# Performance work log

Measured on AMD Instinct MI355X. Metric: run time of the kernel, lower is better.

Reference implementation:

```python
import jax, jax.numpy as jnp
import numpy as np

B, T, DIN, H, DOUT = 64, 1024, 256, 512, 256


def _lstm_layer(xseq, Wih, bih, Whh, bhh):
    """xseq: (T, B, Din) -> hidden sequence (T, B, Hout)."""
    bsz = xseq.shape[1]
    hdim = Whh.shape[0]
    # hoist the input projection out of the recurrence (one big GEMM)
    xg = jnp.einsum('tbd,dh->tbh', xseq, Wih) + bih  # (T, B, 4H)

    def step(carry, xg_t):
        h, c = carry
        gates = xg_t + h @ Whh + bhh          # (B, 4H)
        i, f, g, o = jnp.split(gates, 4, axis=-1)  # torch chunk order: i,f,g,o
        c = jax.nn.sigmoid(f) * c + jax.nn.sigmoid(i) * jnp.tanh(g)
        h = jax.nn.sigmoid(o) * jnp.tanh(c)
        return (h, c), h

    h0 = jnp.zeros((bsz, hdim), xseq.dtype)
    (_, _), hs = jax.lax.scan(step, (h0, h0), xg)
    return hs


def setup_inputs() -> dict:
    key = jax.random.key(0)
    ks = jax.random.split(key, 9)

    def lin(k, fan_in, fan_out):
        bound = 1.0 / np.sqrt(fan_in)
        kw, kb = jax.random.split(k)
        W = jax.random.uniform(kw, (fan_in, fan_out), jnp.float32, -bound, bound)
        b = jax.random.uniform(kb, (fan_out,), jnp.float32, -bound, bound)
        return W, b

    x = jax.random.normal(ks[0], (B, T, DIN), jnp.float32)
    W_ih0, b_ih0 = lin(ks[1], DIN, 4 * H)
    W_hh0, b_hh0 = lin(ks[2], H, 4 * H)
    W_ih1, b_ih1 = lin(ks[3], H, 4 * DOUT)
    W_hh1, b_hh1 = lin(ks[4], DOUT, 4 * DOUT)
    return {
        'x': x,
        'W_ih0': W_ih0, 'b_ih0': b_ih0, 'W_hh0': W_hh0, 'b_hh0': b_hh0,
        'W_ih1': W_ih1, 'b_ih1': b_ih1, 'W_hh1': W_hh1, 'b_hh1': b_hh1,
    }


def reference(x, W_ih0, b_ih0, W_hh0, b_hh0, W_ih1, b_ih1, W_hh1, b_hh1):
    xseq = jnp.transpose(x, (1, 0, 2))              # (T, B, DIN)
    h1 = _lstm_layer(xseq, W_ih0, b_ih0, W_hh0, b_hh0)   # (T, B, H)
    h2 = _lstm_layer(h1, W_ih1, b_ih1, W_hh1, b_hh1)     # (T, B, DOUT)
    return jnp.transpose(h2, (1, 0, 2))             # (B, T, DOUT)
```

## Files before the change

### kernel.cpp

```cpp
#include <hip/hip_runtime.h>


constexpr int BB   = 64;
constexpr int TT   = 1024;
constexpr int DIN  = 256;
constexpr int H0   = 512;
constexpr int H1   = 256;
constexpr int NWG0 = 128;
constexpr int NWG1 = 64;
constexpr int NWG  = NWG0 + NWG1;
constexpr int NTHR = 256;
constexpr int NKT  = 24;

typedef _Float16 v8h __attribute__((ext_vector_type(8)));
typedef __fp16   v2p __attribute__((ext_vector_type(2)));
typedef float    v4f __attribute__((ext_vector_type(4)));
typedef unsigned int v4u __attribute__((ext_vector_type(4)));

union U1 { unsigned u; v2p h; };
union U4 { v4u u; v8h h; };

__device__ __forceinline__ unsigned pk2(float a, float b){
  U1 c; c.h = __builtin_amdgcn_cvt_pkrtz(a, b); return c.u;
}
__device__ __forceinline__ float lo16(unsigned u){ U1 c; c.u = u; return (float)c.h[0]; }
__device__ __forceinline__ float hi16(unsigned u){ U1 c; c.u = u; return (float)c.h[1]; }
__device__ __forceinline__ v8h as_h8(v4u u){ U4 c; c.u = u; return c.h; }

__device__ __forceinline__ v4f mfma16(v8h a, v8h b, v4f c){
  return __builtin_amdgcn_mfma_f32_16x16x32_f16(a, b, c, 0, 0, 0);
}

__device__ __forceinline__ float sigf(float v){ return 1.0f / (1.0f + __expf(-v)); }
__device__ __forceinline__ float tanhf_(float v){
  float e = __expf(2.0f * v);
  return 1.0f - 2.0f / (e + 1.0f);
}

__device__ __forceinline__ void waitflags(const unsigned* f, int n, unsigned tgt, int lane){
  for (;;){
    bool ok = true;
    #pragma unroll
    for (int base = 0; base < n; base += 64)
      ok = ok && (__hip_atomic_load(f + base + lane, __ATOMIC_RELAXED,
                                    __HIP_MEMORY_SCOPE_AGENT) >= tgt);
    if (__all(ok)) return;
    __builtin_amdgcn_s_sleep(1);
  }
}

__device__ __forceinline__ void acq_fence(){
  __builtin_amdgcn_fence(__ATOMIC_ACQUIRE, "agent");
}

__device__ __forceinline__ void frag_from_pairs(v4u p0, v4u p1, v8h& A, v8h& B){
  v4u ua, ub;
  ua[0] = __builtin_amdgcn_perm(p0[1], p0[0], 0x05040100u);
  ua[1] = __builtin_amdgcn_perm(p0[3], p0[2], 0x05040100u);
  ua[2] = __builtin_amdgcn_perm(p1[1], p1[0], 0x05040100u);
  ua[3] = __builtin_amdgcn_perm(p1[3], p1[2], 0x05040100u);
  ub[0] = __builtin_amdgcn_perm(p0[1], p0[0], 0x07060302u);
  ub[1] = __builtin_amdgcn_perm(p0[3], p0[2], 0x07060302u);
  ub[2] = __builtin_amdgcn_perm(p1[1], p1[0], 0x07060302u);
  ub[3] = __builtin_amdgcn_perm(p1[3], p1[2], 0x07060302u);
  A = as_h8(ua); B = as_h8(ub);
}

__device__ __forceinline__ void frag_from_floats(v4f f0, v4f f1, v8h& A, v8h& B){
  float v[8] = { f0[0], f0[1], f0[2], f0[3], f1[0], f1[1], f1[2], f1[3] };
  v4u ua, ub;
  #pragma unroll
  for (int d = 0; d < 4; ++d){
    unsigned p = pk2(v[2*d], v[2*d+1]);
    ua[d] = p;
    ub[d] = pk2(v[2*d] - lo16(p), v[2*d+1] - hi16(p));
  }
  A = as_h8(ua); B = as_h8(ub);
}

__global__ void __launch_bounds__(NTHR, 1)
lstm_mfma(const float* __restrict__ x, const unsigned* __restrict__ xp, int use_xp,
          const float* __restrict__ Wih0, const float* __restrict__ bih0,
          const float* __restrict__ Whh0, const float* __restrict__ bhh0,
          const float* __restrict__ Wih1, const float* __restrict__ bih1,
          const float* __restrict__ Whh1, const float* __restrict__ bhh1,
          unsigned* h1p, unsigned* h2p,
          unsigned* flg, float* out)
{
  __shared__ v4u wfbs[NKT * 64];

  const int tid   = threadIdx.x;
  const int wg    = blockIdx.x;
  const bool isL0 = wg < NWG0;
  const int lw    = isL0 ? wg : wg - NWG0;
  const int H     = isL0 ? H0 : H1;
  const int jbase = lw * 4;
  const int lane  = tid & 63;
  const int mt    = tid >> 6;
  const int n     = lane & 15;
  const int quad  = lane >> 4;
  const int gcol  = (n >> 2) * H + jbase + (n & 3);
  const int brow  = mt * 16 + n;

  v4u wfa[NKT];
  {
    const float* Wi = isL0 ? Wih0 : Wih1;
    const float* Wh = isL0 ? Whh0 : Whh1;
    const int Ki  = isL0 ? DIN : H0;
    const int ldw = 4 * H;
    #pragma unroll
    for (int kt = 0; kt < NKT; ++kt){
      const int ks = kt * 32 + quad * 8;
      float w[8];
      #pragma unroll
      for (int j = 0; j < 8; ++j){
        const int k = ks + j;
        w[j] = (k < Ki) ? Wi[(size_t)k * ldw + gcol]
                        : Wh[(size_t)(k - Ki) * ldw + gcol];
      }
      v4u ua, ub;
      #pragma unroll
      for (int d = 0; d < 4; ++d){
        const unsigned p = pk2(w[2*d], w[2*d+1]);
        ua[d] = p;
        ub[d] = pk2(w[2*d] - lo16(p), w[2*d+1] - hi16(p));
      }
      wfa[kt] = ua;
      if (mt == 0) wfbs[kt * 64 + lane] = ub;
    }
  }
  const float bsum = isL0 ? (bih0[gcol] + bhh0[gcol]) : (bih1[gcol] + bhh1[gcol]);

  float c0 = 0.f, c1 = 0.f, c2 = 0.f, c3 = 0.f;
  __syncthreads();

  for (int i = 0; i <= TT; ++i){
    const bool act = isL0 ? (i < TT) : (i >= 1);
    const int t    = isL0 ? i : (i - 1);

    v4f acc1 = { bsum, bsum, bsum, bsum };
    v4f acc2 = { 0.f, 0.f, 0.f, 0.f };

    if (isL0 && act){
      if (use_xp){
        const unsigned* xr = xp + ((size_t)brow * TT + t) * DIN + quad * 8;
        v4u xP0[8], xP1[8];
        #pragma unroll
        for (int kt = 0; kt < 8; ++kt){
          xP0[kt] = *(const v4u*)(xr + kt * 32);
          xP1[kt] = *(const v4u*)(xr + kt * 32 + 4);
        }
        #pragma unroll
        for (int kt = 0; kt < 8; ++kt){
          v8h A, Ab; frag_from_pairs(xP0[kt], xP1[kt], A, Ab);
          v8h Wa = as_h8(wfa[kt]), Wb = as_h8(wfbs[kt * 64 + lane]);
          acc1 = mfma16(A,  Wa, acc1);
          acc2 = mfma16(A,  Wb, acc2);
          acc2 = mfma16(Ab, Wa, acc2);
        }
      } else {
        const float* xr = x + ((size_t)brow * TT + t) * DIN + quad * 8;
        v4f xF0[8], xF1[8];
        #pragma unroll
        for (int kt = 0; kt < 8; ++kt){
          xF0[kt] = *(const v4f*)(xr + kt * 32);
          xF1[kt] = *(const v4f*)(xr + kt * 32 + 4);
        }
        #pragma unroll
        for (int kt = 0; kt < 8; ++kt){
          v8h A, Ab; frag_from_floats(xF0[kt], xF1[kt], A, Ab);
          v8h Wa = as_h8(wfa[kt]), Wb = as_h8(wfbs[kt * 64 + lane]);
          acc1 = mfma16(A,  Wa, acc1);
          acc2 = mfma16(A,  Wb, acc2);
          acc2 = mfma16(Ab, Wa, acc2);
        }
      }
    }

    if (tid < 64){
      if (i >= 1) waitflags(flg, NWG, (unsigned)i, lane);
      acq_fence();
    }
    __syncthreads();

    if (act){
      if (isL0){
        const unsigned* hr = h1p + (size_t)((t + 1) & 1) * (BB * H0)
                                 + (size_t)brow * H0 + quad * 8;
        v4u hP0[16], hP1[16];
        #pragma unroll
        for (int kt = 0; kt < 16; ++kt){
          hP0[kt] = *(const v4u*)(hr + kt * 32);
          hP1[kt] = *(const v4u*)(hr + kt * 32 + 4);
        }
        #pragma unroll
        for (int kt = 0; kt < 16; ++kt){
          v8h A, Ab; frag_from_pairs(hP0[kt], hP1[kt], A, Ab);
          v8h Wa = as_h8(wfa[kt + 8]), Wb = as_h8(wfbs[(kt + 8) * 64 + lane]);
          acc1 = mfma16(A,  Wa, acc1);
          acc2 = mfma16(A,  Wb, acc2);
          acc2 = mfma16(Ab, Wa, acc2);
        }
      } else {
        const unsigned* h2r = h2p + (size_t)((t + 1) & 1) * (BB * H1)
                                  + (size_t)brow * H1 + quad * 8;
        const unsigned* hr  = h1p + (size_t)(t & 1) * (BB * H0)
                                  + (size_t)brow * H0 + quad * 8;
        v4u aP0[8], aP1[8];
        #pragma unroll
        for (int kt = 0; kt < 8; ++kt){
          aP0[kt] = *(const v4u*)(h2r + kt * 32);
          aP1[kt] = *(const v4u*)(h2r + kt * 32 + 4);
        }
        v4u bP0[16], bP1[16];
        #pragma unroll
        for (int kt = 0; kt < 16; ++kt){
          bP0[kt] = *(const v4u*)(hr + kt * 32);
          bP1[kt] = *(const v4u*)(hr + kt * 32 + 4);
        }
        #pragma unroll
        for (int kt = 0; kt < 8; ++kt){
          v8h A, Ab; frag_from_pairs(aP0[kt], aP1[kt], A, Ab);
          v8h Wa = as_h8(wfa[kt + 16]), Wb = as_h8(wfbs[(kt + 16) * 64 + lane]);
          acc1 = mfma16(A,  Wa, acc1);
          acc2 = mfma16(A,  Wb, acc2);
          acc2 = mfma16(Ab, Wa, acc2);
        }
        #pragma unroll
        for (int kt = 0; kt < 16; ++kt){
          v8h A, Ab; frag_from_pairs(bP0[kt], bP1[kt], A, Ab);
          v8h Wa = as_h8(wfa[kt]), Wb = as_h8(wfbs[kt * 64 + lane]);
          acc1 = mfma16(A,  Wa, acc1);
          acc2 = mfma16(A,  Wb, acc2);
          acc2 = mfma16(Ab, Wa, acc2);
        }
      }

      v4f gv = acc1 + acc2;
      float pv0 = __shfl_xor(gv[0], 4), pv1 = __shfl_xor(gv[1], 4),
            pv2 = __shfl_xor(gv[2], 4), pv3 = __shfl_xor(gv[3], 4);
      float qv0 = __shfl_xor(gv[0], 8), qv1 = __shfl_xor(gv[1], 8),
            qv2 = __shfl_xor(gv[2], 8), qv3 = __shfl_xor(gv[3], 8);
      float sv0 = __shfl_xor(pv0, 8), sv1 = __shfl_xor(pv1, 8),
            sv2 = __shfl_xor(pv2, 8), sv3 = __shfl_xor(pv3, 8);

      if (n < 4){
        float iv[4] = { gv[0], gv[1], gv[2], gv[3] };
        float fv[4] = { pv0, pv1, pv2, pv3 };
        float gg[4] = { qv0, qv1, qv2, qv3 };
        float ov[4] = { sv0, sv1, sv2, sv3 };
        float cc[4] = { c0, c1, c2, c3 };
        const int col = jbase + n;
        #pragma unroll
        for (int r = 0; r < 4; ++r){
          float cn = sigf(fv[r]) * cc[r] + sigf(iv[r]) * tanhf_(gg[r]);
          float hn = sigf(ov[r]) * tanhf_(cn);
          cc[r] = cn;
          const int b = mt * 16 + quad * 4 + r;
          unsigned pa = pk2(hn, 0.f);
          unsigned pd = pk2(hn, hn - lo16(pa));
          if (isL0){
            __hip_atomic_store(h1p + (size_t)(t & 1) * (BB * H0) + (size_t)b * H0 + col,
                               pd, __ATOMIC_RELAXED, __HIP_MEMORY_SCOPE_AGENT);
          } else {
            __hip_atomic_store(h2p + (size_t)(t & 1) * (BB * H1) + (size_t)b * H1 + col,
                               pd, __ATOMIC_RELAXED, __HIP_MEMORY_SCOPE_AGENT);
            __hip_atomic_store(out + ((size_t)b * TT + t) * H1 + col, hn,
                               __ATOMIC_RELAXED, __HIP_MEMORY_SCOPE_AGENT);
          }
        }
        c0 = cc[0]; c1 = cc[1]; c2 = cc[2]; c3 = cc[3];
      }
    }

    __syncthreads();
    if (tid == 0){
      __hip_atomic_store(flg + wg, (unsigned)(i + 1),
                         __ATOMIC_RELAXED, __HIP_MEMORY_SCOPE_AGENT);
    }
  }
}

__global__ void init_ws(unsigned* ws, int nz){
  int i = blockIdx.x * blockDim.x + threadIdx.x;
  if (i < nz)
    __hip_atomic_store(ws + i, 0u, __ATOMIC_RELAXED, __HIP_MEMORY_SCOPE_AGENT);
}

__global__ void conv_x(const float4* __restrict__ x4,
                       unsigned long long* __restrict__ xp2, int n4){
  int i = blockIdx.x * blockDim.x + threadIdx.x;
  if (i >= n4) return;
  float4 f = x4[i];
  float v[4] = { f.x, f.y, f.z, f.w };
  unsigned o[4];
  #pragma unroll
  for (int d = 0; d < 4; ++d){
    unsigned p = pk2(v[d], 0.f);
    o[d] = pk2(v[d], v[d] - lo16(p));
  }
  unsigned long long lo = (unsigned long long)o[0] | ((unsigned long long)o[1] << 32);
  unsigned long long hi = (unsigned long long)o[2] | ((unsigned long long)o[3] << 32);
  __hip_atomic_store(xp2 + 2 * i + 0, lo, __ATOMIC_RELAXED, __HIP_MEMORY_SCOPE_AGENT);
  __hip_atomic_store(xp2 + 2 * i + 1, hi, __ATOMIC_RELAXED, __HIP_MEMORY_SCOPE_AGENT);
}

extern "C" void kernel_launch(void* const* d_in, const int* in_sizes, int n_in,
                              void* d_out, int out_size, void* d_ws, size_t ws_size,
                              hipStream_t stream) {
  const float* x    = (const float*)d_in[0];
  const float* Wih0 = (const float*)d_in[1];
  const float* bih0 = (const float*)d_in[2];
  const float* Whh0 = (const float*)d_in[3];
  const float* bhh0 = (const float*)d_in[4];
  const float* Wih1 = (const float*)d_in[5];
  const float* bih1 = (const float*)d_in[6];
  const float* Whh1 = (const float*)d_in[7];
  const float* bhh1 = (const float*)d_in[8];
  float* outp = (float*)d_out;

  unsigned* ws   = (unsigned*)d_ws;
  unsigned* h1p  = ws;
  unsigned* h2p  = h1p + 2 * BB * H0;
  unsigned* flg  = h2p + 2 * BB * H1;
  unsigned* xp   = flg + 2 * TT;
  const int nz = 2 * BB * H0 + 2 * BB * H1 + 2 * TT;

  const size_t need_xp = ((size_t)nz + (size_t)BB * TT * DIN) * 4;
  int use_xp = (ws_size >= need_xp) ? 1 : 0;

  init_ws<<<dim3((nz + 255) / 256), dim3(256), 0, stream>>>(ws, nz);
  if (use_xp){
    const int n4 = BB * TT * DIN / 4;
    conv_x<<<dim3((n4 + 255) / 256), dim3(256), 0, stream>>>(
        (const float4*)x, (unsigned long long*)xp, n4);
  }

  lstm_mfma<<<dim3(NWG), dim3(NTHR), 0, stream>>>(
      x, xp, use_xp,
      Wih0, bih0, Whh0, bhh0,
      Wih1, bih1, Whh1, bhh1,
      h1p, h2p, flg, outp);
}
```

Measured before the change: 9.227 ms.

## Triple-buffer layer-0 hidden state to relax cross-layer barrier for L0 workgroups

Layer-0 hidden state moves from a double buffer to a triple buffer, so layer-0 workgroups at step i only need layer-1 workgroups to have finished step i-1 rather than step i. This loosens the global flag wait between the two concurrently running layers and shortens the critical path of the per-step grid barrier. Compiler scheduling fences are also placed between the global loads and the MFMA loops so all loads issue before compute. The cost is more workspace and a modulo-3 index per step, and correctness now depends on the buffer-reuse distance being safe.

```diff
diff --git a/kernel.cpp b/kernel.cpp
--- a/kernel.cpp
+++ b/kernel.cpp
@@ -37,13 +37,14 @@
   return 1.0f - 2.0f / (e + 1.0f);
 }
 
-__device__ __forceinline__ void waitflags(const unsigned* f, int n, unsigned tgt, int lane){
+__device__ __forceinline__ void sched_fence(){ asm volatile("" ::: "memory"); }
+
+__device__ __forceinline__ void waitflags2(const unsigned* f, unsigned tgt0,
+                                           unsigned tgt1, int lane){
   for (;;){
-    bool ok = true;
-    #pragma unroll
-    for (int base = 0; base < n; base += 64)
-      ok = ok && (__hip_atomic_load(f + base + lane, __ATOMIC_RELAXED,
-                                    __HIP_MEMORY_SCOPE_AGENT) >= tgt);
+    bool ok = (__hip_atomic_load(f + lane,       __ATOMIC_RELAXED, __HIP_MEMORY_SCOPE_AGENT) >= tgt0)
+           && (__hip_atomic_load(f + 64 + lane,  __ATOMIC_RELAXED, __HIP_MEMORY_SCOPE_AGENT) >= tgt0)
+           && (__hip_atomic_load(f + 128 + lane, __ATOMIC_RELAXED, __HIP_MEMORY_SCOPE_AGENT) >= tgt1);
     if (__all(ok)) return;
     __builtin_amdgcn_s_sleep(1);
   }
@@ -137,6 +138,9 @@
   for (int i = 0; i <= TT; ++i){
     const bool act = isL0 ? (i < TT) : (i >= 1);
     const int t    = isL0 ? i : (i - 1);
+    const int s_w  = ((unsigned)t) % 3u;
+    const int s_r  = ((unsigned)(t + 2)) % 3u;
+    const int s_c  = ((unsigned)t) % 3u;
 
     v4f acc1 = { bsum, bsum, bsum, bsum };
     v4f acc2 = { 0.f, 0.f, 0.f, 0.f };
@@ -150,6 +154,7 @@
           xP0[kt] = *(const v4u*)(xr + kt * 32);
           xP1[kt] = *(const v4u*)(xr + kt * 32 + 4);
         }
+        sched_fence();
         #pragma unroll
         for (int kt = 0; kt < 8; ++kt){
           v8h A, Ab; frag_from_pairs(xP0[kt], xP1[kt], A, Ab);
@@ -166,6 +171,7 @@
           xF0[kt] = *(const v4f*)(xr + kt * 32);
           xF1[kt] = *(const v4f*)(xr + kt * 32 + 4);
         }
+        sched_fence();
         #pragma unroll
         for (int kt = 0; kt < 8; ++kt){
           v8h A, Ab; frag_from_floats(xF0[kt], xF1[kt], A, Ab);
@@ -178,14 +184,17 @@
     }
 
     if (tid < 64){
-      if (i >= 1) waitflags(flg, NWG, (unsigned)i, lane);
+      if (i >= 1){
+        if (isL0) waitflags2(flg, (unsigned)i, (i >= 2) ? (unsigned)(i - 1) : 0u, lane);
+        else      waitflags2(flg, (unsigned)i, (unsigned)i, lane);
+      }
       acq_fence();
     }
     __syncthreads();
 
     if (act){
       if (isL0){
-        const unsigned* hr = h1p + (size_t)((t + 1) & 1) * (BB * H0)
+        const unsigned* hr = h1p + (size_t)s_r * (BB * H0)
                                  + (size_t)brow * H0 + quad * 8;
         v4u hP0[16], hP1[16];
         #pragma unroll
@@ -193,6 +202,7 @@
           hP0[kt] = *(const v4u*)(hr + kt * 32);
           hP1[kt] = *(const v4u*)(hr + kt * 32 + 4);
         }
+        sched_fence();
         #pragma unroll
         for (int kt = 0; kt < 16; ++kt){
           v8h A, Ab; frag_from_pairs(hP0[kt], hP1[kt], A, Ab);
@@ -204,7 +214,7 @@
       } else {
         const unsigned* h2r = h2p + (size_t)((t + 1) & 1) * (BB * H1)
                                   + (size_t)brow * H1 + quad * 8;
-        const unsigned* hr  = h1p + (size_t)(t & 1) * (BB * H0)
+        const unsigned* hr  = h1p + (size_t)s_c * (BB * H0)
                                   + (size_t)brow * H0 + quad * 8;
         v4u aP0[8], aP1[8];
         #pragma unroll
@@ -218,6 +228,7 @@
           bP0[kt] = *(const v4u*)(hr + kt * 32);
           bP1[kt] = *(const v4u*)(hr + kt * 32 + 4);
         }
+        sched_fence();
         #pragma unroll
         for (int kt = 0; kt < 8; ++kt){
           v8h A, Ab; frag_from_pairs(aP0[kt], aP1[kt], A, Ab);
@@ -260,7 +271,7 @@
           unsigned pa = pk2(hn, 0.f);
           unsigned pd = pk2(hn, hn - lo16(pa));
           if (isL0){
-            __hip_atomic_store(h1p + (size_t)(t & 1) * (BB * H0) + (size_t)b * H0 + col,
+            __hip_atomic_store(h1p + (size_t)s_w * (BB * H0) + (size_t)b * H0 + col,
                                pd, __ATOMIC_RELAXED, __HIP_MEMORY_SCOPE_AGENT);
           } else {
             __hip_atomic_store(h2p + (size_t)(t & 1) * (BB * H1) + (size_t)b * H1 + col,
@@ -321,10 +332,10 @@
 
   unsigned* ws   = (unsigned*)d_ws;
   unsigned* h1p  = ws;
-  unsigned* h2p  = h1p + 2 * BB * H0;
+  unsigned* h2p  = h1p + 3 * BB * H0;
   unsigned* flg  = h2p + 2 * BB * H1;
   unsigned* xp   = flg + 2 * TT;
-  const int nz = 2 * BB * H0 + 2 * BB * H1 + 2 * TT;
+  const int nz = 3 * BB * H0 + 2 * BB * H1 + 2 * TT;
 
   const size_t need_xp = ((size_t)nz + (size_t)BB * TT * DIN) * 4;
   int use_xp = (ws_size >= need_xp) ? 1 : 0;
```

Result: no change. 9.285 ms (+0.6%).
